# Optimization experiments

Measured on AMD Instinct MI355X. Metric: run time of the kernel, lower is better.

## Reference

```python
import jax, jax.numpy as jnp
import numpy as np

N_RAYS = 32768
N_SAMPLES = N_RAYS * 32  # 1,048,576
FDIM = 32
HID = 64
RGB_HID = 64
THRESHOLD = 1e-4  # early_termination_threshold


def setup_inputs() -> dict:
    key = jax.random.key(0)
    ks = jax.random.split(key, 12)
    # ragged per-ray sample counts (avg 32), adjusted so total is exactly N_SAMPLES
    rng = np.random.default_rng(0)
    counts = rng.integers(8, 57, size=N_RAYS)
    delta = int(N_SAMPLES - counts.sum())
    if delta >= 0:
        counts[:delta] += 1
    else:
        counts[:(-delta)] -= 1
    starts = np.concatenate([[0], np.cumsum(counts)[:-1]])
    packing_info = jnp.asarray(np.stack([starts, counts], axis=1), dtype=jnp.int32)
    ray_ids = jnp.asarray(np.repeat(np.arange(N_RAYS), counts), dtype=jnp.int32)

    pos = jax.random.uniform(ks[0], (N_SAMPLES, 3), minval=-1.0, maxval=1.0)
    dirs = jax.random.normal(ks[1], (N_SAMPLES, 3))
    dirs = dirs / jnp.linalg.norm(dirs, axis=1, keepdims=True)
    dt = jax.random.uniform(ks[2], (N_SAMPLES, 1), minval=0.0, maxval=0.01)
    packed_samples = jnp.concatenate([pos, dirs, dt], axis=1)

    def lin(k, fi, fo):
        return jax.random.normal(k, (fi, fo)) / np.sqrt(fi)

    return {
        "packed_samples": packed_samples,
        "packing_info": packing_info,
        "ray_ids": ray_ids,
        "w1": lin(ks[3], 3, HID), "b1": jnp.zeros(HID),
        "w2": lin(ks[4], HID, FDIM), "b2": jnp.zeros(FDIM),
        "w_sigma": lin(ks[5], FDIM, 1), "b_sigma": jnp.zeros(1),
        "w_rgb1": lin(ks[6], FDIM + 3, RGB_HID), "b_rgb1": jnp.zeros(RGB_HID),
        "w_rgb2": lin(ks[7], RGB_HID, 3), "b_rgb2": jnp.zeros(3),
        "bg_color": jnp.ones(3),
    }


def reference(packed_samples, packing_info, ray_ids, w1, b1, w2, b2,
              w_sigma, b_sigma, w_rgb1, b_rgb1, w_rgb2, b_rgb2, bg_color):
    pos = packed_samples[:, :3]
    dirs = packed_samples[:, 3:6]
    dt = packed_samples[:, 6]

    # feature_module
    feats = jax.nn.relu(pos @ w1 + b1) @ w2 + b2            # [N, FDIM]
    # sigma_decoder
    sigma = jax.nn.softplus(feats @ w_sigma + b_sigma)[:, 0]  # [N]

    # NerfWeights: per-ray transmittance T_i = exp(-sum_{j<i in ray} sigma_j*dt_j),
    # weight_i = T_i * (1 - exp(-sigma_i*dt_i)), zeroed once T drops below threshold.
    tau = sigma * dt
    c_excl = jnp.cumsum(tau) - tau                           # exclusive global cumsum
    seg_base = c_excl[packing_info[:, 0]]                    # cumsum before each ray's start
    T = jnp.exp(-(c_excl - seg_base[ray_ids]))
    alpha = 1.0 - jnp.exp(-tau)
    weights = jnp.where(T > THRESHOLD, T * alpha, 0.0)       # [N]

    # rgb_decoder (masked gather in torch is a perf trick; weight==0 kills masked rgbs)
    h = jax.nn.relu(jnp.concatenate([feats, dirs], axis=1) @ w_rgb1 + b_rgb1)
    rgbs = jax.nn.sigmoid(h @ w_rgb2 + b_rgb2)               # [N, 3]

    contrib = rgbs * weights[:, None]
    rendered = jax.ops.segment_sum(contrib, ray_ids, num_segments=N_RAYS)   # [n_rays,3]
    opac = jax.ops.segment_sum(weights, ray_ids, num_segments=N_RAYS)       # [n_rays]
    return rendered + bg_color * (1.0 - opac[:, None])
```

## Files before the change

### kernel.cpp

```cpp
#include <hip/hip_runtime.h>
#include <hip/hip_bf16.h>
#include <math.h>
#include <stdint.h>

#define N_RAYS    32768
#define N_SAMPLES (N_RAYS * 32)
#define THRESH 0.0001f
#define TBL_OFF  (16u * 1024u * 1024u)

typedef __attribute__((ext_vector_type(8))) __bf16 bf16x8;
typedef __attribute__((ext_vector_type(4))) float  f32x4;
typedef float f4a __attribute__((ext_vector_type(4), aligned(4)));

union FragU { __hip_bfloat162 h2[4]; uint32_t w[4]; bf16x8 v; };
union RecU  { bf16x8 v; f32x4 f; uint4 u; };

__device__ inline __hip_bfloat162 pk2(float lo, float hi) {
    float2 t; t.x = lo; t.y = hi;
    return __float22bfloat162_rn(t);
}

__device__ inline bf16x8 pack8(const float* vals) {
    FragU u;
    u.h2[0] = pk2(vals[0], vals[1]);
    u.h2[1] = pk2(vals[2], vals[3]);
    u.h2[2] = pk2(vals[4], vals[5]);
    u.h2[3] = pk2(vals[6], vals[7]);
    return u.v;
}

__device__ inline float rcp_fast(float x) {
    float r;
    asm("v_rcp_f32 %0, %1" : "=v"(r) : "v"(x));
    return r;
}
__device__ inline float sigmoid_fast(float x) { return rcp_fast(1.0f + __expf(-x)); }
__device__ inline float softplus_fast(float x) {
    const float e = __expf(-fabsf(x));
    return fmaxf(x, 0.0f) + __logf(1.0f + e);
}

__global__ __launch_bounds__(256) void nerf_build_frags(
    const float* __restrict__ w1,  const float* __restrict__ b1,
    const float* __restrict__ w2,  const float* __restrict__ b2,
    const float* __restrict__ w_sigma, const float* __restrict__ b_sigma,
    const float* __restrict__ w_rgb1,  const float* __restrict__ b_rgb1,
    const float* __restrict__ w_rgb2,  const float* __restrict__ b_rgb2,
    uint4* __restrict__ tbl)
{
    const int wid  = threadIdx.x >> 6;
    const int lane = threadIdx.x & 63;
    const int g    = lane >> 4;
    const int sl   = lane & 15;
    RecU rec;

    if (wid == 0) {
        #pragma unroll
        for (int t = 0; t < 4; ++t) {
            float v[8] = {0,0,0,0,0,0,0,0};
            if (g == 0) {
                const int j = t*16 + sl;
                v[0] = w1[j]; v[1] = w1[64+j]; v[2] = w1[128+j]; v[3] = b1[j];
            }
            rec.v = pack8(v); tbl[t*64 + lane] = rec.u;
        }
        #pragma unroll
        for (int t = 0; t < 2; ++t)
            #pragma unroll
            for (int c = 0; c < 2; ++c) {
                float v[8];
                #pragma unroll
                for (int q = 0; q < 8; ++q) {
                    const int j = 16*(2*c + (q>>2)) + 4*g + (q&3);
                    v[q] = w2[j*32 + t*16 + sl];
                }
                rec.v = pack8(v); tbl[(4 + 2*t + c)*64 + lane] = rec.u;
            }
    } else if (wid == 1) {
        #pragma unroll
        for (int t = 0; t < 4; ++t) {
            float v[8];
            #pragma unroll
            for (int q = 0; q < 8; ++q) {
                const int f = 16*(q>>2) + 4*g + (q&3);
                v[q] = w_rgb1[f*64 + t*16 + sl];
            }
            rec.v = pack8(v); tbl[(8 + t)*64 + lane] = rec.u;
        }
        #pragma unroll
        for (int t = 0; t < 4; ++t) {
            float v[8] = {0,0,0,0,0,0,0,0};
            if (g == 0) {
                const int j = t*16 + sl;
                v[4] = w_rgb1[32*64 + j]; v[5] = w_rgb1[33*64 + j];
                v[6] = w_rgb1[34*64 + j]; v[7] = b_rgb1[j];
            }
            rec.v = pack8(v); tbl[(12 + t)*64 + lane] = rec.u;
        }
    } else if (wid == 2) {
        #pragma unroll
        for (int c = 0; c < 2; ++c) {
            float v[8];
            #pragma unroll
            for (int q = 0; q < 8; ++q) {
                const int hh = 16*(2*c + (q>>2)) + 4*g + (q&3);
                v[q] = (sl < 3) ? w_rgb2[hh*3 + sl] : 0.0f;
            }
            rec.v = pack8(v); tbl[(16 + c)*64 + lane] = rec.u;
        }
        {
            float v[8];
            #pragma unroll
            for (int q = 0; q < 8; ++q) {
                const int f = 16*(q>>2) + 4*g + (q&3);
                v[q] = (sl == 3) ? w_sigma[f] : 0.0f;
            }
            rec.v = pack8(v); tbl[18*64 + lane] = rec.u;
        }
        #pragma unroll
        for (int t = 0; t < 2; ++t) {
            #pragma unroll
            for (int r = 0; r < 4; ++r) rec.f[r] = b2[16*t + 4*g + r];
            tbl[(19 + t)*64 + lane] = rec.u;
        }
        {
            rec.f[0] = b_rgb2[0]; rec.f[1] = b_rgb2[1];
            rec.f[2] = b_rgb2[2]; rec.f[3] = b_sigma[0];
            tbl[21*64 + lane] = rec.u;
        }
    }
}

__global__ __launch_bounds__(256, 3) void nerf_mlp_mfma(
    const float* __restrict__ samples,
    const uint4* __restrict__ tbl,
    float4* __restrict__ out)
{
    const int lane = threadIdx.x & 63;
    const int g    = lane >> 4;
    const int sl   = lane & 15;
    const int wgid = (blockIdx.x * blockDim.x + threadIdx.x) >> 6;
    const int base0 = wgid * 128;

    f4a sa[2], sb[2];
    {
        const float* sp = samples + (size_t)(base0 + sl) * 7;
        sa[0] = *(const f4a*)sp;  sb[0] = *(const f4a*)(sp + 3);
    }

    bf16x8 A1[4], A2[2][2], Ar1a[4], Ar1b[4], Ar2[2], Ar2f;
    f32x4 b2i[2], arinit;
    {
        RecU r_;
        #pragma unroll
        for (int t = 0; t < 4; ++t) { r_.u = tbl[t*64 + lane];       A1[t]   = r_.v; }
        #pragma unroll
        for (int t = 0; t < 2; ++t)
            #pragma unroll
            for (int c = 0; c < 2; ++c) { r_.u = tbl[(4+2*t+c)*64 + lane]; A2[t][c] = r_.v; }
        #pragma unroll
        for (int t = 0; t < 4; ++t) { r_.u = tbl[(8+t)*64 + lane];   Ar1a[t] = r_.v; }
        #pragma unroll
        for (int t = 0; t < 4; ++t) { r_.u = tbl[(12+t)*64 + lane];  Ar1b[t] = r_.v; }
        #pragma unroll
        for (int c = 0; c < 2; ++c) { r_.u = tbl[(16+c)*64 + lane];  Ar2[c]  = r_.v; }
        r_.u = tbl[18*64 + lane]; Ar2f = r_.v;
        r_.u = tbl[19*64 + lane]; b2i[0] = r_.f;
        r_.u = tbl[20*64 + lane]; b2i[1] = r_.f;
        r_.u = tbl[21*64 + lane]; arinit = r_.f;
    }

    const float biasone = (g == 0) ? 1.0f : 0.0f;
    const f32x4 zero4 = {0.f, 0.f, 0.f, 0.f};

    #pragma unroll
    for (int it = 0; it < 8; ++it) {
        const int cb = it & 1;
        const int nb = (it + 1) & 1;
        if (it < 7) {
            const float* sp = samples + (size_t)(base0 + (it + 1) * 16 + sl) * 7;
            sa[nb] = *(const f4a*)sp;  sb[nb] = *(const f4a*)(sp + 3);
        }

        FragU bin;
        bin.h2[0] = pk2(sa[cb].x, sa[cb].y);
        bin.h2[1] = pk2(sa[cb].z, biasone);
        bin.h2[2] = pk2(sb[cb].x, sb[cb].y);
        bin.h2[3] = pk2(sb[cb].z, biasone);

        f32x4 accL1[4];
        #pragma unroll
        for (int t = 0; t < 4; ++t)
            accL1[t] = __builtin_amdgcn_mfma_f32_16x16x32_bf16(A1[t], bin.v, zero4, 0,0,0);

        FragU B2c[2];
        #pragma unroll
        for (int c = 0; c < 2; ++c) {
            B2c[c].h2[0] = pk2(fmaxf(accL1[2*c  ][0],0.f), fmaxf(accL1[2*c  ][1],0.f));
            B2c[c].h2[1] = pk2(fmaxf(accL1[2*c  ][2],0.f), fmaxf(accL1[2*c  ][3],0.f));
            B2c[c].h2[2] = pk2(fmaxf(accL1[2*c+1][0],0.f), fmaxf(accL1[2*c+1][1],0.f));
            B2c[c].h2[3] = pk2(fmaxf(accL1[2*c+1][2],0.f), fmaxf(accL1[2*c+1][3],0.f));
        }

        f32x4 accL2[2];
        #pragma unroll
        for (int t = 0; t < 2; ++t) {
            accL2[t] = __builtin_amdgcn_mfma_f32_16x16x32_bf16(A2[t][0], B2c[0].v, b2i[t], 0,0,0);
            accL2[t] = __builtin_amdgcn_mfma_f32_16x16x32_bf16(A2[t][1], B2c[1].v, accL2[t], 0,0,0);
        }
        FragU Bf;
        Bf.h2[0] = pk2(accL2[0][0], accL2[0][1]);
        Bf.h2[1] = pk2(accL2[0][2], accL2[0][3]);
        Bf.h2[2] = pk2(accL2[1][0], accL2[1][1]);
        Bf.h2[3] = pk2(accL2[1][2], accL2[1][3]);

        f32x4 ah[4];
        #pragma unroll
        for (int t = 0; t < 4; ++t) {
            ah[t] = __builtin_amdgcn_mfma_f32_16x16x32_bf16(Ar1a[t], Bf.v, zero4, 0,0,0);
            ah[t] = __builtin_amdgcn_mfma_f32_16x16x32_bf16(Ar1b[t], bin.v, ah[t], 0,0,0);
        }
        FragU Bh[2];
        #pragma unroll
        for (int c = 0; c < 2; ++c) {
            Bh[c].h2[0] = pk2(fmaxf(ah[2*c  ][0],0.f), fmaxf(ah[2*c  ][1],0.f));
            Bh[c].h2[1] = pk2(fmaxf(ah[2*c  ][2],0.f), fmaxf(ah[2*c  ][3],0.f));
            Bh[c].h2[2] = pk2(fmaxf(ah[2*c+1][0],0.f), fmaxf(ah[2*c+1][1],0.f));
            Bh[c].h2[3] = pk2(fmaxf(ah[2*c+1][2],0.f), fmaxf(ah[2*c+1][3],0.f));
        }

        f32x4 ar;
        ar = __builtin_amdgcn_mfma_f32_16x16x32_bf16(Ar2[0], Bh[0].v, arinit, 0,0,0);
        ar = __builtin_amdgcn_mfma_f32_16x16x32_bf16(Ar2[1], Bh[1].v, ar, 0,0,0);
        ar = __builtin_amdgcn_mfma_f32_16x16x32_bf16(Ar2f,   Bf.v,    ar, 0,0,0);

        const float rr    = sigmoid_fast(ar[0]);
        const float gg    = sigmoid_fast(ar[1]);
        const float bb    = sigmoid_fast(ar[2]);
        const float sigma = softplus_fast(ar[3]);
        const float tau   = sigma * sb[cb].w;
        if (g == 0) out[base0 + it * 16 + sl] = make_float4(tau, rr, gg, bb);
    }
}

__global__ __launch_bounds__(256) void nerf_render_kernel(
    const float4* __restrict__ smp,
    const int*    __restrict__ packing,
    const float*  __restrict__ bg,
    float*        __restrict__ out)
{
    const int gtid = blockIdx.x * blockDim.x + threadIdx.x;
    const int ray  = gtid >> 6;
    const int lane = threadIdx.x & 63;
    if (ray >= N_RAYS) return;

    const int start = packing[2 * ray];
    const int count = packing[2 * ray + 1];

    float tau = 0.0f, r = 0.0f, g = 0.0f, b = 0.0f;
    if (lane < count) {
        const float4 v = smp[start + lane];
        tau = v.x; r = v.y; g = v.z; b = v.w;
    }

    float incl = tau;
    #pragma unroll
    for (int off = 1; off < 64; off <<= 1) {
        const float v = __shfl_up(incl, off, 64);
        if (lane >= off) incl += v;
    }
    const float c_excl = incl - tau;

    const float T     = __expf(-c_excl);
    const float alpha = 1.0f - __expf(-tau);
    float w = (lane < count && T > THRESH) ? T * alpha : 0.0f;

    float cr = r * w, cg = g * w, cb = b * w;

    #pragma unroll
    for (int off = 32; off > 0; off >>= 1) {
        cr += __shfl_down(cr, off, 64);
        cg += __shfl_down(cg, off, 64);
        cb += __shfl_down(cb, off, 64);
        w  += __shfl_down(w,  off, 64);
    }

    if (lane == 0) {
        out[ray * 3 + 0] = cr + bg[0] * (1.0f - w);
        out[ray * 3 + 1] = cg + bg[1] * (1.0f - w);
        out[ray * 3 + 2] = cb + bg[2] * (1.0f - w);
    }
}

extern "C" void kernel_launch(void* const* d_in, const int* in_sizes, int n_in,
                              void* d_out, int out_size, void* d_ws, size_t ws_size,
                              hipStream_t stream) {
    const float* samples  = (const float*)d_in[0];
    const int*   packing  = (const int*)  d_in[1];
    const float* w1       = (const float*)d_in[3];
    const float* b1       = (const float*)d_in[4];
    const float* w2       = (const float*)d_in[5];
    const float* b2       = (const float*)d_in[6];
    const float* w_sigma  = (const float*)d_in[7];
    const float* b_sigma  = (const float*)d_in[8];
    const float* w_rgb1   = (const float*)d_in[9];
    const float* b_rgb1   = (const float*)d_in[10];
    const float* w_rgb2   = (const float*)d_in[11];
    const float* b_rgb2   = (const float*)d_in[12];
    const float* bg       = (const float*)d_in[13];

    float4* smp = (float4*)d_ws;
    uint4*  tbl = (uint4*)((char*)d_ws + TBL_OFF);
    float*  out = (float*)d_out;

    nerf_build_frags<<<1, 256, 0, stream>>>(
        w1, b1, w2, b2, w_sigma, b_sigma,
        w_rgb1, b_rgb1, w_rgb2, b_rgb2, tbl);

    nerf_mlp_mfma<<<2048, 256, 0, stream>>>(samples, tbl, (float4*)smp);

    nerf_render_kernel<<<(N_RAYS * 64) / 256, 256, 0, stream>>>(smp, packing, bg, out);
}
```

Baseline: 48.74 us.

## Switch MLP from 16x16x32 to 32x32x16 bf16 MFMA tiles

Rewrites the per-sample MLP to use 32x32x16 MFMA instructions, processing 32 samples per tile and 256 samples per wave, with the weight fragment table relaid out to match. Layer 1 packs position and direction into half the K dimension and zero-pads the rest. The larger tiles cut the instruction count and per-sample fragment packing. In exchange each wave uses more accumulator registers, so occupancy drops to 2 blocks per SM and only half as many blocks launch. The padded K in layer 1 also wastes some MFMA work.

```diff
diff --git a/kernel.cpp b/kernel.cpp
--- a/kernel.cpp
+++ b/kernel.cpp
@@ -8,12 +8,22 @@
 #define THRESH 0.0001f
 #define TBL_OFF  (16u * 1024u * 1024u)
 
-typedef __attribute__((ext_vector_type(8))) __bf16 bf16x8;
-typedef __attribute__((ext_vector_type(4))) float  f32x4;
+#define R_A1   0
+#define R_A2   2
+#define R_R1A  6
+#define R_R1B  10
+#define R_AR2  12
+#define R_AR2F 16
+#define R_B2I  18
+#define R_ARI  22
+
+typedef __attribute__((ext_vector_type(8)))  __bf16 bf16x8;
+typedef __attribute__((ext_vector_type(16))) float  f32x16;
 typedef float f4a __attribute__((ext_vector_type(4), aligned(4)));
 
-union FragU { __hip_bfloat162 h2[4]; uint32_t w[4]; bf16x8 v; };
-union RecU  { bf16x8 v; f32x4 f; uint4 u; };
+union FragU  { __hip_bfloat162 h2[4]; uint32_t w[4]; bf16x8 v; };
+union RecU   { bf16x8 v; uint4 u; };
+union Rec16U { f32x16 v; uint4 u[4]; float f[16]; };
 
 __device__ inline __hip_bfloat162 pk2(float lo, float hi) {
     float2 t; t.x = lo; t.y = hi;
@@ -38,6 +48,25 @@
 __device__ inline float softplus_fast(float x) {
     const float e = __expf(-fabsf(x));
     return fmaxf(x, 0.0f) + __logf(1.0f + e);
+}
+
+template <int P>
+__device__ inline bf16x8 packB_relu(f32x16 a) {
+    FragU u;
+    u.h2[0] = pk2(fmaxf(a[P+0],0.f), fmaxf(a[P+1],0.f));
+    u.h2[1] = pk2(fmaxf(a[P+2],0.f), fmaxf(a[P+3],0.f));
+    u.h2[2] = pk2(fmaxf(a[P+4],0.f), fmaxf(a[P+5],0.f));
+    u.h2[3] = pk2(fmaxf(a[P+6],0.f), fmaxf(a[P+7],0.f));
+    return u.v;
+}
+template <int P>
+__device__ inline bf16x8 packB_plain(f32x16 a) {
+    FragU u;
+    u.h2[0] = pk2(a[P+0], a[P+1]);
+    u.h2[1] = pk2(a[P+2], a[P+3]);
+    u.h2[2] = pk2(a[P+4], a[P+5]);
+    u.h2[3] = pk2(a[P+6], a[P+7]);
+    return u.v;
 }
 
 __global__ __launch_bounds__(256) void nerf_build_frags(
@@ -50,20 +79,31 @@
 {
     const int wid  = threadIdx.x >> 6;
     const int lane = threadIdx.x & 63;
-    const int g    = lane >> 4;
-    const int sl   = lane & 15;
+    const int m    = lane & 31;
+    const int h    = lane >> 5;
     RecU rec;
 
     if (wid == 0) {
         #pragma unroll
-        for (int t = 0; t < 4; ++t) {
+        for (int t = 0; t < 2; ++t) {
             float v[8] = {0,0,0,0,0,0,0,0};
-            if (g == 0) {
-                const int j = t*16 + sl;
+            if (h == 0) {
+                const int j = 32*t + m;
                 v[0] = w1[j]; v[1] = w1[64+j]; v[2] = w1[128+j]; v[3] = b1[j];
             }
-            rec.v = pack8(v); tbl[t*64 + lane] = rec.u;
-        }
+            rec.v = pack8(v); tbl[(R_A1+t)*64 + lane] = rec.u;
+        }
+        #pragma unroll
+        for (int c = 0; c < 4; ++c) {
+            float v[8];
+            #pragma unroll
+            for (int q = 0; q < 8; ++q) {
+                const int j = 16*c + (q&3) + 8*(q>>2) + 4*h;
+                v[q] = w2[j*32 + m];
+            }
+            rec.v = pack8(v); tbl[(R_A2+c)*64 + lane] = rec.u;
+        }
+    } else if (wid == 1) {
         #pragma unroll
         for (int t = 0; t < 2; ++t)
             #pragma unroll
@@ -71,175 +111,170 @@
                 float v[8];
                 #pragma unroll
                 for (int q = 0; q < 8; ++q) {
-                    const int j = 16*(2*c + (q>>2)) + 4*g + (q&3);
-                    v[q] = w2[j*32 + t*16 + sl];
+                    const int f = 16*c + (q&3) + 8*(q>>2) + 4*h;
+                    v[q] = w_rgb1[f*64 + 32*t + m];
                 }
-                rec.v = pack8(v); tbl[(4 + 2*t + c)*64 + lane] = rec.u;
-            }
-    } else if (wid == 1) {
-        #pragma unroll
-        for (int t = 0; t < 4; ++t) {
+                rec.v = pack8(v); tbl[(R_R1A+2*t+c)*64 + lane] = rec.u;
+            }
+        #pragma unroll
+        for (int t = 0; t < 2; ++t) {
+            float v[8] = {0,0,0,0,0,0,0,0};
+            if (h == 1) {
+                const int j = 32*t + m;
+                v[0] = w_rgb1[32*64 + j]; v[1] = w_rgb1[33*64 + j];
+                v[2] = w_rgb1[34*64 + j]; v[3] = b_rgb1[j];
+            }
+            rec.v = pack8(v); tbl[(R_R1B+t)*64 + lane] = rec.u;
+        }
+    } else if (wid == 2) {
+        #pragma unroll
+        for (int c = 0; c < 4; ++c) {
             float v[8];
             #pragma unroll
             for (int q = 0; q < 8; ++q) {
-                const int f = 16*(q>>2) + 4*g + (q&3);
-                v[q] = w_rgb1[f*64 + t*16 + sl];
-            }
-            rec.v = pack8(v); tbl[(8 + t)*64 + lane] = rec.u;
-        }
-        #pragma unroll
-        for (int t = 0; t < 4; ++t) {
-            float v[8] = {0,0,0,0,0,0,0,0};
-            if (g == 0) {
-                const int j = t*16 + sl;
-                v[4] = w_rgb1[32*64 + j]; v[5] = w_rgb1[33*64 + j];
-                v[6] = w_rgb1[34*64 + j]; v[7] = b_rgb1[j];
-            }
-            rec.v = pack8(v); tbl[(12 + t)*64 + lane] = rec.u;
-        }
-    } else if (wid == 2) {
+                const int hh = 16*c + (q&3) + 8*(q>>2) + 4*h;
+                v[q] = (m < 3) ? w_rgb2[hh*3 + m] : 0.0f;
+            }
+            rec.v = pack8(v); tbl[(R_AR2+c)*64 + lane] = rec.u;
+        }
         #pragma unroll
         for (int c = 0; c < 2; ++c) {
             float v[8];
             #pragma unroll
             for (int q = 0; q < 8; ++q) {
-                const int hh = 16*(2*c + (q>>2)) + 4*g + (q&3);
-                v[q] = (sl < 3) ? w_rgb2[hh*3 + sl] : 0.0f;
-            }
-            rec.v = pack8(v); tbl[(16 + c)*64 + lane] = rec.u;
-        }
-        {
-            float v[8];
-            #pragma unroll
-            for (int q = 0; q < 8; ++q) {
-                const int f = 16*(q>>2) + 4*g + (q&3);
-                v[q] = (sl == 3) ? w_sigma[f] : 0.0f;
-            }
-            rec.v = pack8(v); tbl[18*64 + lane] = rec.u;
-        }
-        #pragma unroll
-        for (int t = 0; t < 2; ++t) {
-            #pragma unroll
-            for (int r = 0; r < 4; ++r) rec.f[r] = b2[16*t + 4*g + r];
-            tbl[(19 + t)*64 + lane] = rec.u;
-        }
-        {
-            rec.f[0] = b_rgb2[0]; rec.f[1] = b_rgb2[1];
-            rec.f[2] = b_rgb2[2]; rec.f[3] = b_sigma[0];
-            tbl[21*64 + lane] = rec.u;
-        }
-    }
-}
-
-__global__ __launch_bounds__(256, 3) void nerf_mlp_mfma(
+                const int f = 16*c + (q&3) + 8*(q>>2) + 4*h;
+                v[q] = (m == 3) ? w_sigma[f] : 0.0f;
+            }
+            rec.v = pack8(v); tbl[(R_AR2F+c)*64 + lane] = rec.u;
+        }
+        Rec16U r16;
+        #pragma unroll
+        for (int i = 0; i < 4; ++i) {
+            #pragma unroll
+            for (int e = 0; e < 4; ++e) r16.f[4*i+e] = b2[e + 8*i + 4*h];
+        }
+        #pragma unroll
+        for (int i = 0; i < 4; ++i) tbl[(R_B2I+i)*64 + lane] = r16.u[i];
+        #pragma unroll
+        for (int i = 0; i < 4; ++i) {
+            #pragma unroll
+            for (int e = 0; e < 4; ++e) {
+                const int r = e + 8*i + 4*h;
+                r16.f[4*i+e] = (r < 3) ? b_rgb2[r] : ((r == 3) ? b_sigma[0] : 0.0f);
+            }
+        }
+        #pragma unroll
+        for (int i = 0; i < 4; ++i) tbl[(R_ARI+i)*64 + lane] = r16.u[i];
+    }
+}
+
+__global__ __launch_bounds__(256, 2) void nerf_mlp_mfma(
     const float* __restrict__ samples,
     const uint4* __restrict__ tbl,
     float4* __restrict__ out)
 {
     const int lane = threadIdx.x & 63;
-    const int g    = lane >> 4;
-    const int sl   = lane & 15;
+    const int m32  = lane & 31;
+    const int h    = lane >> 5;
     const int wgid = (blockIdx.x * blockDim.x + threadIdx.x) >> 6;
-    const int base0 = wgid * 128;
+    const int base0 = wgid * 256;
 
     f4a sa[2], sb[2];
     {
-        const float* sp = samples + (size_t)(base0 + sl) * 7;
+        const float* sp = samples + (size_t)(base0 + m32) * 7;
         sa[0] = *(const f4a*)sp;  sb[0] = *(const f4a*)(sp + 3);
     }
 
-    bf16x8 A1[4], A2[2][2], Ar1a[4], Ar1b[4], Ar2[2], Ar2f;
-    f32x4 b2i[2], arinit;
+    bf16x8 A1[2], A2[4], R1a[4], R1b[2], Ar2[4], Ar2f[2];
+    f32x16 b2i, arinit;
     {
         RecU r_;
         #pragma unroll
-        for (int t = 0; t < 4; ++t) { r_.u = tbl[t*64 + lane];       A1[t]   = r_.v; }
-        #pragma unroll
-        for (int t = 0; t < 2; ++t)
-            #pragma unroll
-            for (int c = 0; c < 2; ++c) { r_.u = tbl[(4+2*t+c)*64 + lane]; A2[t][c] = r_.v; }
-        #pragma unroll
-        for (int t = 0; t < 4; ++t) { r_.u = tbl[(8+t)*64 + lane];   Ar1a[t] = r_.v; }
-        #pragma unroll
-        for (int t = 0; t < 4; ++t) { r_.u = tbl[(12+t)*64 + lane];  Ar1b[t] = r_.v; }
-        #pragma unroll
-        for (int c = 0; c < 2; ++c) { r_.u = tbl[(16+c)*64 + lane];  Ar2[c]  = r_.v; }
-        r_.u = tbl[18*64 + lane]; Ar2f = r_.v;
-        r_.u = tbl[19*64 + lane]; b2i[0] = r_.f;
-        r_.u = tbl[20*64 + lane]; b2i[1] = r_.f;
-        r_.u = tbl[21*64 + lane]; arinit = r_.f;
-    }
-
-    const float biasone = (g == 0) ? 1.0f : 0.0f;
-    const f32x4 zero4 = {0.f, 0.f, 0.f, 0.f};
+        for (int t = 0; t < 2; ++t) { r_.u = tbl[(R_A1+t)*64 + lane];  A1[t]  = r_.v; }
+        #pragma unroll
+        for (int c = 0; c < 4; ++c) { r_.u = tbl[(R_A2+c)*64 + lane];  A2[c]  = r_.v; }
+        #pragma unroll
+        for (int i = 0; i < 4; ++i) { r_.u = tbl[(R_R1A+i)*64 + lane]; R1a[i] = r_.v; }
+        #pragma unroll
+        for (int t = 0; t < 2; ++t) { r_.u = tbl[(R_R1B+t)*64 + lane]; R1b[t] = r_.v; }
+        #pragma unroll
+        for (int c = 0; c < 4; ++c) { r_.u = tbl[(R_AR2+c)*64 + lane]; Ar2[c] = r_.v; }
+        #pragma unroll
+        for (int c = 0; c < 2; ++c) { r_.u = tbl[(R_AR2F+c)*64 + lane]; Ar2f[c] = r_.v; }
+        Rec16U r16;
+        #pragma unroll
+        for (int i = 0; i < 4; ++i) r16.u[i] = tbl[(R_B2I+i)*64 + lane];
+        b2i = r16.v;
+        #pragma unroll
+        for (int i = 0; i < 4; ++i) r16.u[i] = tbl[(R_ARI+i)*64 + lane];
+        arinit = r16.v;
+    }
+
+    const f32x16 zero16 = {0,0,0,0,0,0,0,0,0,0,0,0,0,0,0,0};
 
     #pragma unroll
     for (int it = 0; it < 8; ++it) {
         const int cb = it & 1;
         const int nb = (it + 1) & 1;
         if (it < 7) {
-            const float* sp = samples + (size_t)(base0 + (it + 1) * 16 + sl) * 7;
+            const float* sp = samples + (size_t)(base0 + (it + 1) * 32 + m32) * 7;
             sa[nb] = *(const f4a*)sp;  sb[nb] = *(const f4a*)(sp + 3);
         }
 
         FragU bin;
-        bin.h2[0] = pk2(sa[cb].x, sa[cb].y);
-        bin.h2[1] = pk2(sa[cb].z, biasone);
-        bin.h2[2] = pk2(sb[cb].x, sb[cb].y);
-        bin.h2[3] = pk2(sb[cb].z, biasone);
-
-        f32x4 accL1[4];
-        #pragma unroll
-        for (int t = 0; t < 4; ++t)
-            accL1[t] = __builtin_amdgcn_mfma_f32_16x16x32_bf16(A1[t], bin.v, zero4, 0,0,0);
-
-        FragU B2c[2];
-        #pragma unroll
-        for (int c = 0; c < 2; ++c) {
-            B2c[c].h2[0] = pk2(fmaxf(accL1[2*c  ][0],0.f), fmaxf(accL1[2*c  ][1],0.f));
-            B2c[c].h2[1] = pk2(fmaxf(accL1[2*c  ][2],0.f), fmaxf(accL1[2*c  ][3],0.f));
-            B2c[c].h2[2] = pk2(fmaxf(accL1[2*c+1][0],0.f), fmaxf(accL1[2*c+1][1],0.f));
-            B2c[c].h2[3] = pk2(fmaxf(accL1[2*c+1][2],0.f), fmaxf(accL1[2*c+1][3],0.f));
-        }
-
-        f32x4 accL2[2];
+        bin.h2[0] = pk2(h ? sb[cb].x : sa[cb].x, h ? sb[cb].y : sa[cb].y);
+        bin.h2[1] = pk2(h ? sb[cb].z : sa[cb].z, 1.0f);
+        bin.w[2] = 0; bin.w[3] = 0;
+
+        f32x16 accL1[2];
+        #pragma unroll
+        for (int t = 0; t < 2; ++t)
+            accL1[t] = __builtin_amdgcn_mfma_f32_32x32x16_bf16(A1[t], bin.v, zero16, 0,0,0);
+
+        bf16x8 B2c[4];
+        B2c[0] = packB_relu<0>(accL1[0]);
+        B2c[1] = packB_relu<8>(accL1[0]);
+        B2c[2] = packB_relu<0>(accL1[1]);
+        B2c[3] = packB_relu<8>(accL1[1]);
+
+        f32x16 accL2;
+        accL2 = __builtin_amdgcn_mfma_f32_32x32x16_bf16(A2[0], B2c[0], b2i, 0,0,0);
+        accL2 = __builtin_amdgcn_mfma_f32_32x32x16_bf16(A2[1], B2c[1], accL2, 0,0,0);
+        accL2 = __builtin_amdgcn_mfma_f32_32x32x16_bf16(A2[2], B2c[2], accL2, 0,0,0);
+        accL2 = __builtin_amdgcn_mfma_f32_32x32x16_bf16(A2[3], B2c[3], accL2, 0,0,0);
+
+        bf16x8 Bf[2];
+        Bf[0] = packB_plain<0>(accL2);
+        Bf[1] = packB_plain<8>(accL2);
+
+        f32x16 ah[2];
         #pragma unroll
         for (int t = 0; t < 2; ++t) {
-            accL2[t] = __builtin_amdgcn_mfma_f32_16x16x32_bf16(A2[t][0], B2c[0].v, b2i[t], 0,0,0);
-            accL2[t] = __builtin_amdgcn_mfma_f32_16x16x32_bf16(A2[t][1], B2c[1].v, accL2[t], 0,0,0);
-        }
-        FragU Bf;
-        Bf.h2[0] = pk2(accL2[0][0], accL2[0][1]);
-        Bf.h2[1] = pk2(accL2[0][2], accL2[0][3]);
-        Bf.h2[2] = pk2(accL2[1][0], accL2[1][1]);
-        Bf.h2[3] = pk2(accL2[1][2], accL2[1][3]);
-
-        f32x4 ah[4];
-        #pragma unroll
-        for (int t = 0; t < 4; ++t) {
-            ah[t] = __builtin_amdgcn_mfma_f32_16x16x32_bf16(Ar1a[t], Bf.v, zero4, 0,0,0);
-            ah[t] = __builtin_amdgcn_mfma_f32_16x16x32_bf16(Ar1b[t], bin.v, ah[t], 0,0,0);
-        }
-        FragU Bh[2];
-        #pragma unroll
-        for (int c = 0; c < 2; ++c) {
-            Bh[c].h2[0] = pk2(fmaxf(ah[2*c  ][0],0.f), fmaxf(ah[2*c  ][1],0.f));
-            Bh[c].h2[1] = pk2(fmaxf(ah[2*c  ][2],0.f), fmaxf(ah[2*c  ][3],0.f));
-            Bh[c].h2[2] = pk2(fmaxf(ah[2*c+1][0],0.f), fmaxf(ah[2*c+1][1],0.f));
-            Bh[c].h2[3] = pk2(fmaxf(ah[2*c+1][2],0.f), fmaxf(ah[2*c+1][3],0.f));
-        }
-
-        f32x4 ar;
-        ar = __builtin_amdgcn_mfma_f32_16x16x32_bf16(Ar2[0], Bh[0].v, arinit, 0,0,0);
-        ar = __builtin_amdgcn_mfma_f32_16x16x32_bf16(Ar2[1], Bh[1].v, ar, 0,0,0);
-        ar = __builtin_amdgcn_mfma_f32_16x16x32_bf16(Ar2f,   Bf.v,    ar, 0,0,0);
+            ah[t] = __builtin_amdgcn_mfma_f32_32x32x16_bf16(R1a[2*t+0], Bf[0], zero16, 0,0,0);
+            ah[t] = __builtin_amdgcn_mfma_f32_32x32x16_bf16(R1a[2*t+1], Bf[1], ah[t], 0,0,0);
+            ah[t] = __builtin_amdgcn_mfma_f32_32x32x16_bf16(R1b[t],     bin.v, ah[t], 0,0,0);
+        }
+
+        bf16x8 Bh[4];
+        Bh[0] = packB_relu<0>(ah[0]);
+        Bh[1] = packB_relu<8>(ah[0]);
+        Bh[2] = packB_relu<0>(ah[1]);
+        Bh[3] = packB_relu<8>(ah[1]);
+
+        f32x16 ar;
+        ar = __builtin_amdgcn_mfma_f32_32x32x16_bf16(Ar2[0], Bh[0], arinit, 0,0,0);
+        ar = __builtin_amdgcn_mfma_f32_32x32x16_bf16(Ar2[1], Bh[1], ar, 0,0,0);
+        ar = __builtin_amdgcn_mfma_f32_32x32x16_bf16(Ar2[2], Bh[2], ar, 0,0,0);
+        ar = __builtin_amdgcn_mfma_f32_32x32x16_bf16(Ar2[3], Bh[3], ar, 0,0,0);
+        ar = __builtin_amdgcn_mfma_f32_32x32x16_bf16(Ar2f[0], Bf[0], ar, 0,0,0);
+        ar = __builtin_amdgcn_mfma_f32_32x32x16_bf16(Ar2f[1], Bf[1], ar, 0,0,0);
 
         const float rr    = sigmoid_fast(ar[0]);
         const float gg    = sigmoid_fast(ar[1]);
         const float bb    = sigmoid_fast(ar[2]);
         const float sigma = softplus_fast(ar[3]);
         const float tau   = sigma * sb[cb].w;
-        if (g == 0) out[base0 + it * 16 + sl] = make_float4(tau, rr, gg, bb);
+        if (lane < 32) out[base0 + it * 32 + m32] = make_float4(tau, rr, gg, bb);
     }
 }
 
@@ -317,7 +352,7 @@
         w1, b1, w2, b2, w_sigma, b_sigma,
         w_rgb1, b_rgb1, w_rgb2, b_rgb2, tbl);
 
-    nerf_mlp_mfma<<<2048, 256, 0, stream>>>(samples, tbl, (float4*)smp);
+    nerf_mlp_mfma<<<1024, 256, 0, stream>>>(samples, tbl, (float4*)smp);
 
     nerf_render_kernel<<<(N_RAYS * 64) / 256, 256, 0, stream>>>(smp, packing, bg, out);
 }
```

After: 47.54 us. 2.5% less time.
